# Optimization experiments

Hardware: AMD Instinct MI355X
Metric: run time of the kernel (lower is better)

Reference implementation:

```python
import jax, jax.numpy as jnp
import numpy as np

N_NODES = 50000
N_EDGES = 1600000
N_GRAPHS = 64
F_IN = 256
H = 1024
EPS = 1e-5


def setup_inputs() -> dict:
    key = jax.random.key(0)
    ks = jax.random.split(key, 6)
    x = jax.random.normal(ks[0], (N_NODES, F_IN), dtype=jnp.float32)
    edge_index = jax.random.randint(ks[1], (2, N_EDGES), 0, N_NODES, dtype=jnp.int32)
    batch = jnp.sort(jax.random.randint(ks[2], (N_NODES,), 0, N_GRAPHS, dtype=jnp.int32))
    # Glorot-ish init for GCN weights
    W0 = jax.random.normal(ks[3], (F_IN, H), dtype=jnp.float32) * (1.0 / np.sqrt(F_IN))
    b0 = jnp.zeros((H,), dtype=jnp.float32)
    Ws = jax.random.normal(ks[4], (3, H, H), dtype=jnp.float32) * (1.0 / np.sqrt(H))
    bs = jnp.zeros((3, H), dtype=jnp.float32)
    gammas = jnp.ones((4, H), dtype=jnp.float32)
    betas = jnp.zeros((4, H), dtype=jnp.float32)
    return {"x": x, "edge_index": edge_index, "batch": batch,
            "W0": W0, "b0": b0, "Ws": Ws, "bs": bs,
            "gammas": gammas, "betas": betas}


def _gcn_norm(edge_index, n_nodes):
    # Add self-loops (PyG GCNConv default), compute symmetric normalization.
    loops = jnp.arange(n_nodes, dtype=edge_index.dtype)
    row = jnp.concatenate([edge_index[0], loops])  # sources
    col = jnp.concatenate([edge_index[1], loops])  # targets (aggregation index)
    ones = jnp.ones(row.shape[0], dtype=jnp.float32)
    deg = jax.ops.segment_sum(ones, col, num_segments=n_nodes)
    dinv = jnp.where(deg > 0, jax.lax.rsqrt(deg), 0.0)
    norm = dinv[row] * dinv[col]  # [E + N]
    return row, col, norm


def _layer(h, W, b, gamma, beta, row, col, norm):
    ht = h @ W                                           # [N, H] GEMM
    msg = ht[row] * norm[:, None]                        # gather + scale
    agg = jax.ops.segment_sum(msg, col, num_segments=N_NODES) + b
    mu = jnp.mean(agg, axis=-1, keepdims=True)
    var = jnp.mean(jnp.square(agg - mu), axis=-1, keepdims=True)
    hn = (agg - mu) * jax.lax.rsqrt(var + EPS) * gamma + beta
    return jax.nn.relu(hn)


def reference(x, edge_index, batch, W0, b0, Ws, bs, gammas, betas):
    row, col, norm = _gcn_norm(edge_index, N_NODES)
    h = _layer(x, W0, b0, gammas[0], betas[0], row, col, norm)
    for i in range(3):
        h = _layer(h, Ws[i], bs[i], gammas[i + 1], betas[i + 1], row, col, norm)
    # scatter_mean over batch (graph-level pooling)
    sums = jax.ops.segment_sum(h, batch, num_segments=N_GRAPHS)
    cnt = jax.ops.segment_sum(jnp.ones((N_NODES,), jnp.float32), batch, num_segments=N_GRAPHS)
    return sums / jnp.maximum(cnt, 1.0)[:, None]
```

## Files before the change

### kernel.cpp

```cpp
#include <hip/hip_runtime.h>
#include <hip/hip_bf16.h>
#include <stdint.h>

#define NN 50000
#define NE 1600000
#define NG 64
#define FIN 256
#define HD 1024
#define EPSV 1e-5f

typedef __bf16 bf16;
typedef __bf16 bf16x4 __attribute__((ext_vector_type(4)));
typedef __bf16 bf16x8 __attribute__((ext_vector_type(8)));
typedef float f32x4 __attribute__((ext_vector_type(4)));

typedef const __attribute__((address_space(1))) void* gptr_as1;
typedef __attribute__((address_space(3))) void* lptr_as3;

__device__ __forceinline__ void load_g2l_16(const void* g, const void* l) {
  __builtin_amdgcn_global_load_lds((gptr_as1)(uintptr_t)g,
                                   (lptr_as3)(uint32_t)(uintptr_t)l, 16, 0, 0);
}

__global__ void hist_kernel(const int* __restrict__ col, int* __restrict__ cnt, int E) {
  int e = blockIdx.x * 256 + threadIdx.x;
  if (e < E) atomicAdd(&cnt[col[e]], 1);
}

__global__ void dinv_kernel(const int* __restrict__ cnt, float* __restrict__ dinv, int n) {
  int i = blockIdx.x * 256 + threadIdx.x;
  if (i < n) dinv[i] = rsqrtf((float)(cnt[i] + 1));
}

__global__ void scan_partial_kernel(const int* __restrict__ cnt, int* __restrict__ partial, int n) {
  __shared__ int red[4];
  int i = blockIdx.x * 256 + threadIdx.x;
  int v = (i < n) ? cnt[i] : 0;
  #pragma unroll
  for (int off = 32; off; off >>= 1) v += __shfl_down(v, off, 64);
  if ((threadIdx.x & 63) == 0) red[threadIdx.x >> 6] = v;
  __syncthreads();
  if (threadIdx.x == 0) partial[blockIdx.x] = red[0] + red[1] + red[2] + red[3];
}

__global__ void scan_scan_kernel(int* __restrict__ partial, int nb) {
  __shared__ int s[256];
  int t = threadIdx.x;
  int v = (t < nb) ? partial[t] : 0;
  s[t] = v;
  __syncthreads();
  for (int off = 1; off < 256; off <<= 1) {
    int x = (t >= off) ? s[t - off] : 0;
    __syncthreads();
    s[t] += x;
    __syncthreads();
  }
  if (t < nb) partial[t] = s[t] - v;
}

__global__ void scan_final_kernel(const int* __restrict__ cnt, const int* __restrict__ partial,
                                  int* __restrict__ row_ptr, int n, int E) {
  __shared__ int s[256];
  int t = threadIdx.x;
  int i = blockIdx.x * 256 + t;
  int v = (i < n) ? cnt[i] : 0;
  s[t] = v;
  __syncthreads();
  for (int off = 1; off < 256; off <<= 1) {
    int x = (t >= off) ? s[t - off] : 0;
    __syncthreads();
    s[t] += x;
    __syncthreads();
  }
  if (i < n) row_ptr[i] = partial[blockIdx.x] + s[t] - v;
  if (i == 0) row_ptr[n] = E;
}

__global__ void scatter_kernel(const int* __restrict__ rowi, const int* __restrict__ coli,
                               const int* __restrict__ row_ptr, int* __restrict__ fill,
                               const float* __restrict__ dinv,
                               int* __restrict__ csr_src, float* __restrict__ csr_w, int E) {
  int e = blockIdx.x * 256 + threadIdx.x;
  if (e >= E) return;
  int s = rowi[e], d = coli[e];
  int pos = row_ptr[d] + atomicAdd(&fill[d], 1);
  csr_src[pos] = s;
  csr_w[pos] = dinv[s] * dinv[d];
}

__global__ void cvt_kernel(const float* __restrict__ in, bf16* __restrict__ out, int n4) {
  int i = blockIdx.x * 256 + threadIdx.x;
  if (i >= n4) return;
  float4 v = ((const float4*)in)[i];
  bf16x4 o = { (bf16)v.x, (bf16)v.y, (bf16)v.z, (bf16)v.w };
  ((bf16x4*)out)[i] = o;
}

__global__ void transpose_w_kernel(const float* __restrict__ W, bf16* __restrict__ Wt,
                                   int K, int N) {
  __shared__ float tile[32][33];
  int n0 = blockIdx.x * 32, k0 = blockIdx.y * 32;
  int tx = threadIdx.x, ty = threadIdx.y;
  #pragma unroll
  for (int i = ty; i < 32; i += 8) tile[i][tx] = W[(size_t)(k0 + i) * N + n0 + tx];
  __syncthreads();
  #pragma unroll
  for (int i = ty; i < 32; i += 8) Wt[(size_t)(n0 + i) * K + k0 + tx] = (bf16)tile[tx][i];
}

__global__ __launch_bounds__(256, 2) void gemm_bt_q8_kernel(
    const bf16* __restrict__ A, const bf16* __restrict__ Bt,
    uint8_t* __restrict__ C8, float* __restrict__ scales, int M, int K) {
  __shared__ __align__(16) bf16 As[2][128 * 32];
  __shared__ __align__(16) bf16 Bs[2][128 * 32];
  __shared__ float smax[2][128];
  const int tid = threadIdx.x;
  const int w = tid >> 6, l = tid & 63;

  const int nwg = gridDim.x;
  const int o = blockIdx.x;
  const int lid = (o & 7) * (nwg >> 3) + (o >> 3);
  const int m0 = (lid >> 3) * 128, n0 = (lid & 7) * 128;
  const int cb = lid & 7;
  const int wr = w >> 1, wc = w & 1;

  f32x4 acc[4][4] = {};

  const int r0 = tid >> 2;
  const int c8 = (tid & 3) * 8;
  int ar0 = m0 + r0;       if (ar0 >= M) ar0 = M - 1;
  int ar1 = m0 + r0 + 64;  if (ar1 >= M) ar1 = M - 1;
  const bf16* a0 = A + (size_t)ar0 * K + c8;
  const bf16* a1 = A + (size_t)ar1 * K + c8;
  const bf16* b0 = Bt + (size_t)(n0 + r0) * K + c8;
  const bf16* b1 = Bt + (size_t)(n0 + r0 + 64) * K + c8;

  const int mrow = l & 15;
  const int kch = (l >> 4) * 8;

  auto stage = [&](int b, int k) {
    bf16* asw = &As[b][w * 512];
    bf16* bsw = &Bs[b][w * 512];
    load_g2l_16(a0 + k, asw);
    load_g2l_16(a1 + k, asw + 2048);
    load_g2l_16(b0 + k, bsw);
    load_g2l_16(b1 + k, bsw + 2048);
  };

  const int nit = K >> 5;
  stage(0, 0);
  __syncthreads();

  int cur = 0;
  for (int t = 0; t < nit; ++t) {
    if (t + 1 < nit) stage(cur ^ 1, (t + 1) << 5);
    bf16x8 af[4], bf_[4];
    #pragma unroll
    for (int m = 0; m < 4; m++)
      af[m] = *(const bf16x8*)&As[cur][(wr * 64 + m * 16 + mrow) * 32 + kch];
    #pragma unroll
    for (int n = 0; n < 4; n++)
      bf_[n] = *(const bf16x8*)&Bs[cur][(wc * 64 + n * 16 + mrow) * 32 + kch];
    #pragma unroll
    for (int m = 0; m < 4; m++)
      #pragma unroll
      for (int n = 0; n < 4; n++)
        acc[m][n] = __builtin_amdgcn_mfma_f32_16x16x32_bf16(af[m], bf_[n], acc[m][n], 0, 0, 0);
    __syncthreads();
    cur ^= 1;
  }

  float pmax[4][4];
  #pragma unroll
  for (int m = 0; m < 4; m++)
    #pragma unroll
    for (int r = 0; r < 4; r++) {
      float v = 0.f;
      #pragma unroll
      for (int n = 0; n < 4; n++) v = fmaxf(v, fabsf(acc[m][n][r]));
      #pragma unroll
      for (int mask = 1; mask < 16; mask <<= 1) v = fmaxf(v, __shfl_xor(v, mask, 64));
      pmax[m][r] = v;
    }
  if ((l & 15) == 0) {
    #pragma unroll
    for (int m = 0; m < 4; m++)
      #pragma unroll
      for (int r = 0; r < 4; r++)
        smax[wc][wr * 64 + m * 16 + (l >> 4) * 4 + r] = pmax[m][r];
  }
  __syncthreads();

  #pragma unroll
  for (int m = 0; m < 4; m++) {
    #pragma unroll
    for (int r = 0; r < 4; r++) {
      int rl = wr * 64 + m * 16 + (l >> 4) * 4 + r;
      int grow = m0 + rl;
      float mx = fmaxf(smax[0][rl], smax[1][rl]);
      float inv = (mx > 0.f) ? 127.0f / mx : 0.f;
      if (grow < M) {
        if (wc == 0 && (l & 15) == 0)
          scales[(size_t)grow * 8 + cb] = (mx > 0.f) ? mx / 127.0f : 0.f;
        #pragma unroll
        for (int n = 0; n < 4; n++) {
          int gcol = n0 + wc * 64 + n * 16 + (l & 15);
          int u = __float2int_rn(acc[m][n][r] * inv) + 128;
          C8[(size_t)grow * HD + gcol] = (uint8_t)u;
        }
      }
    }
  }
}

__device__ __forceinline__ void acc_u8(float acc[8], float& sw, float w, uint2 d) {
  sw += w;
  acc[0] += w * (float)(d.x & 0xffu);
  acc[1] += w * (float)((d.x >> 8) & 0xffu);
  acc[2] += w * (float)((d.x >> 16) & 0xffu);
  acc[3] += w * (float)(d.x >> 24);
  acc[4] += w * (float)(d.y & 0xffu);
  acc[5] += w * (float)((d.y >> 8) & 0xffu);
  acc[6] += w * (float)((d.y >> 16) & 0xffu);
  acc[7] += w * (float)(d.y >> 24);
}

__global__ __launch_bounds__(256) void agg_ln_u8_kernel(
    const uint8_t* __restrict__ htu8, const float* __restrict__ scales,
    const int* __restrict__ row_ptr,
    const int* __restrict__ csr_src, const float* __restrict__ csr_w,
    const float* __restrict__ dinv, const float* __restrict__ bias,
    const float* __restrict__ gamma, const float* __restrict__ beta,
    bf16* __restrict__ hout) {
  const int g = threadIdx.x >> 7;
  const int node = blockIdx.x * 2 + g;
  const int tt = threadIdx.x & 127;
  const int cbL = tt >> 4;
  const int wid = threadIdx.x >> 6;
  __shared__ float red[4];

  float acc[8] = {};
  float sw = 0.f;

  float dn = dinv[node];
  float wself = dn * dn * scales[(size_t)node * 8 + cbL];
  acc_u8(acc, sw, wself, ((const uint2*)(htu8 + (size_t)node * HD))[tt]);

  int e = row_ptr[node];
  const int e1 = row_ptr[node + 1];
  for (; e + 4 <= e1; e += 4) {
    int s0 = csr_src[e], s1 = csr_src[e + 1], s2 = csr_src[e + 2], s3 = csr_src[e + 3];
    float w0 = csr_w[e] * scales[(size_t)s0 * 8 + cbL];
    float w1 = csr_w[e + 1] * scales[(size_t)s1 * 8 + cbL];
    float w2 = csr_w[e + 2] * scales[(size_t)s2 * 8 + cbL];
    float w3 = csr_w[e + 3] * scales[(size_t)s3 * 8 + cbL];
    uint2 d0 = ((const uint2*)(htu8 + (size_t)s0 * HD))[tt];
    uint2 d1 = ((const uint2*)(htu8 + (size_t)s1 * HD))[tt];
    uint2 d2 = ((const uint2*)(htu8 + (size_t)s2 * HD))[tt];
    uint2 d3 = ((const uint2*)(htu8 + (size_t)s3 * HD))[tt];
    acc_u8(acc, sw, w0, d0);
    acc_u8(acc, sw, w1, d1);
    acc_u8(acc, sw, w2, d2);
    acc_u8(acc, sw, w3, d3);
  }
  for (; e < e1; e++) {
    int src = csr_src[e];
    float wgt = csr_w[e] * scales[(size_t)src * 8 + cbL];
    acc_u8(acc, sw, wgt, ((const uint2*)(htu8 + (size_t)src * HD))[tt]);
  }

  const float4* bias2 = (const float4*)bias;
  float4 ba = bias2[tt * 2], bb = bias2[tt * 2 + 1];
  float c128 = 128.0f * sw;
  acc[0] += ba.x - c128; acc[1] += ba.y - c128; acc[2] += ba.z - c128; acc[3] += ba.w - c128;
  acc[4] += bb.x - c128; acc[5] += bb.y - c128; acc[6] += bb.z - c128; acc[7] += bb.w - c128;

  float s = 0.f;
  #pragma unroll
  for (int j = 0; j < 8; j++) s += acc[j];
  #pragma unroll
  for (int off = 32; off; off >>= 1) s += __shfl_down(s, off, 64);
  if ((threadIdx.x & 63) == 0) red[wid] = s;
  __syncthreads();
  float mean = (red[g * 2] + red[g * 2 + 1]) * (1.0f / HD);
  __syncthreads();

  float d[8], s2 = 0.f;
  #pragma unroll
  for (int j = 0; j < 8; j++) { d[j] = acc[j] - mean; s2 += d[j] * d[j]; }
  #pragma unroll
  for (int off = 32; off; off >>= 1) s2 += __shfl_down(s2, off, 64);
  if ((threadIdx.x & 63) == 0) red[wid] = s2;
  __syncthreads();
  float var = (red[g * 2] + red[g * 2 + 1]) * (1.0f / HD);
  float rstd = rsqrtf(var + EPSV);

  const float4* gam2 = (const float4*)gamma;
  const float4* bet2 = (const float4*)beta;
  float4 g0 = gam2[tt * 2], g1 = gam2[tt * 2 + 1];
  float4 be0 = bet2[tt * 2], be1 = bet2[tt * 2 + 1];
  float gv[8] = {g0.x, g0.y, g0.z, g0.w, g1.x, g1.y, g1.z, g1.w};
  float bv[8] = {be0.x, be0.y, be0.z, be0.w, be1.x, be1.y, be1.z, be1.w};
  bf16x8 o;
  #pragma unroll
  for (int j = 0; j < 8; j++) o[j] = (bf16)fmaxf(d[j] * rstd * gv[j] + bv[j], 0.0f);
  ((bf16x8*)(hout + (size_t)node * HD))[tt] = o;
}

__global__ void starts_kernel(const int* __restrict__ batch, int* __restrict__ start,
                              int n, int ngraph) {
  int g = blockIdx.x * blockDim.x + threadIdx.x;
  if (g > ngraph) return;
  int lo = 0, hi = n;
  while (lo < hi) {
    int mid = (lo + hi) >> 1;
    if (batch[mid] < g) lo = mid + 1; else hi = mid;
  }
  start[g] = lo;
}

#define POOL_CHUNKS 8
__global__ void pool_partial_kernel(const bf16* __restrict__ h, const int* __restrict__ start,
                                    float* __restrict__ out) {
  int g = blockIdx.y, c = blockIdx.x;
  int t = threadIdx.x;
  int s0 = start[g], s1 = start[g + 1];
  int len = s1 - s0;
  int per = (len + POOL_CHUNKS - 1) / POOL_CHUNKS;
  int a = s0 + c * per;
  int b = min(a + per, s1);
  if (a >= b) return;
  f32x4 acc = {0.f, 0.f, 0.f, 0.f};
  for (int n = a; n < b; n++) {
    bf16x4 v = ((const bf16x4*)(h + (size_t)n * HD))[t];
    acc[0] += (float)v[0]; acc[1] += (float)v[1];
    acc[2] += (float)v[2]; acc[3] += (float)v[3];
  }
  float* o = out + (size_t)g * HD + t * 4;
  atomicAdd(o + 0, acc[0]);
  atomicAdd(o + 1, acc[1]);
  atomicAdd(o + 2, acc[2]);
  atomicAdd(o + 3, acc[3]);
}

__global__ void pool_div_kernel(float* __restrict__ out, const int* __restrict__ start) {
  int i = blockIdx.x * 256 + threadIdx.x;
  if (i >= NG * HD) return;
  int g = i >> 10;
  float c = (float)max(start[g + 1] - start[g], 1);
  out[i] = out[i] / c;
}

extern "C" void kernel_launch(void* const* d_in, const int* in_sizes, int n_in,
                              void* d_out, int out_size, void* d_ws, size_t ws_size,
                              hipStream_t stream) {
  const float* x      = (const float*)d_in[0];
  const int*   eidx   = (const int*)d_in[1];
  const int*   batch  = (const int*)d_in[2];
  const float* W0     = (const float*)d_in[3];
  const float* b0     = (const float*)d_in[4];
  const float* Ws     = (const float*)d_in[5];
  const float* bs     = (const float*)d_in[6];
  const float* gammas = (const float*)d_in[7];
  const float* betas  = (const float*)d_in[8];
  float* out = (float*)d_out;

  const int* erow = eidx;
  const int* ecol = eidx + NE;

  char* ws = (char*)d_ws;
  size_t off = 0;
  auto alloc = [&](size_t bytes) {
    void* p = ws + off;
    off = (off + bytes + 255) & ~(size_t)255;
    return p;
  };
  int*     cnt     = (int*)alloc((size_t)NN * 4);
  int*     row_ptr = (int*)alloc((size_t)(NN + 1) * 4);
  int*     fill    = (int*)alloc((size_t)NN * 4);
  int*     partial = (int*)alloc(256 * 4);
  float*   dinv    = (float*)alloc((size_t)NN * 4);
  int*     csr_src = (int*)alloc((size_t)NE * 4);
  float*   csr_w   = (float*)alloc((size_t)NE * 4);
  bf16*    Wt      = (bf16*)alloc((size_t)HD * HD * 2);
  bf16*    hbuf    = (bf16*)alloc((size_t)NN * HD * 2);
  uint8_t* ht8     = (uint8_t*)alloc((size_t)NN * HD);
  float*   scales  = (float*)alloc((size_t)NN * 8 * 4);
  int*     gstart  = (int*)alloc(65 * 4);

  hipMemsetAsync(cnt, 0, (size_t)NN * 4, stream);
  hipMemsetAsync(fill, 0, (size_t)NN * 4, stream);
  hipMemsetAsync(out, 0, (size_t)NG * HD * 4, stream);

  hist_kernel<<<(NE + 255) / 256, 256, 0, stream>>>(ecol, cnt, NE);
  dinv_kernel<<<(NN + 255) / 256, 256, 0, stream>>>(cnt, dinv, NN);
  int nb = (NN + 255) / 256;
  scan_partial_kernel<<<nb, 256, 0, stream>>>(cnt, partial, NN);
  scan_scan_kernel<<<1, 256, 0, stream>>>(partial, nb);
  scan_final_kernel<<<nb, 256, 0, stream>>>(cnt, partial, row_ptr, NN, NE);
  scatter_kernel<<<(NE + 255) / 256, 256, 0, stream>>>(erow, ecol, row_ptr, fill, dinv,
                                                       csr_src, csr_w, NE);
  starts_kernel<<<1, 128, 0, stream>>>(batch, gstart, NN, NG);

  cvt_kernel<<<(NN * FIN / 4 + 255) / 256, 256, 0, stream>>>(x, hbuf, NN * FIN / 4);

  const int nmt = (NN + 127) / 128;
  for (int L = 0; L < 4; L++) {
    int K = (L == 0) ? FIN : HD;
    const float* W    = (L == 0) ? W0 : Ws + (size_t)(L - 1) * HD * HD;
    const float* bias = (L == 0) ? b0 : bs + (size_t)(L - 1) * HD;
    transpose_w_kernel<<<dim3(HD / 32, K / 32), dim3(32, 8), 0, stream>>>(W, Wt, K, HD);
    gemm_bt_q8_kernel<<<nmt * 8, 256, 0, stream>>>(hbuf, Wt, ht8, scales, NN, K);
    agg_ln_u8_kernel<<<NN / 2, 256, 0, stream>>>(ht8, scales, row_ptr, csr_src, csr_w,
                                                 dinv, bias, gammas + (size_t)L * HD,
                                                 betas + (size_t)L * HD, hbuf);
  }

  pool_partial_kernel<<<dim3(POOL_CHUNKS, NG), 256, 0, stream>>>(hbuf, gstart, out);
  pool_div_kernel<<<(NG * HD + 255) / 256, 256, 0, stream>>>(out, gstart);
}
```

Before: 1.681 ms.

## Switch GEMM to int8 MFMA with per-row activation and per-column weight quantization

Quantizes input features, layer activations, and weights to int8, with per-row activation scales and per-column weight scales. The GEMM then runs on the i8 MFMA with int32 accumulation and is dequantized in the epilogue. The aggregation/LayerNorm kernel now emits int8 rows plus a scale, and pooling reads that format. This halves activation storage and traffic and uses the higher-throughput int8 matrix path, but adds extra weight-prep launches and accuracy risk from coarser quantization.

```diff
diff --git a/kernel.cpp b/kernel.cpp
--- a/kernel.cpp
+++ b/kernel.cpp
@@ -10,9 +10,8 @@
 #define EPSV 1e-5f
 
 typedef __bf16 bf16;
-typedef __bf16 bf16x4 __attribute__((ext_vector_type(4)));
-typedef __bf16 bf16x8 __attribute__((ext_vector_type(8)));
 typedef float f32x4 __attribute__((ext_vector_type(4)));
+typedef int i32x4 __attribute__((ext_vector_type(4)));
 
 typedef const __attribute__((address_space(1))) void* gptr_as1;
 typedef __attribute__((address_space(3))) void* lptr_as3;
@@ -88,16 +87,55 @@
   csr_w[pos] = dinv[s] * dinv[d];
 }
 
-__global__ void cvt_kernel(const float* __restrict__ in, bf16* __restrict__ out, int n4) {
-  int i = blockIdx.x * 256 + threadIdx.x;
-  if (i >= n4) return;
-  float4 v = ((const float4*)in)[i];
-  bf16x4 o = { (bf16)v.x, (bf16)v.y, (bf16)v.z, (bf16)v.w };
-  ((bf16x4*)out)[i] = o;
-}
-
-__global__ void transpose_w_kernel(const float* __restrict__ W, bf16* __restrict__ Wt,
-                                   int K, int N) {
+__global__ __launch_bounds__(256) void quant_x_kernel(const float* __restrict__ x,
+                                                      int8_t* __restrict__ A8,
+                                                      float* __restrict__ hscale) {
+  int row = blockIdx.x * 4 + (threadIdx.x >> 6);
+  int t = threadIdx.x & 63;
+  float4 v = ((const float4*)(x + (size_t)row * FIN))[t];
+  float m = fmaxf(fmaxf(fabsf(v.x), fabsf(v.y)), fmaxf(fabsf(v.z), fabsf(v.w)));
+  #pragma unroll
+  for (int off = 32; off; off >>= 1) m = fmaxf(m, __shfl_xor(m, off, 64));
+  float inv = (m > 0.f) ? 127.0f / m : 0.f;
+  int q0 = min(127, max(-127, __float2int_rn(v.x * inv)));
+  int q1 = min(127, max(-127, __float2int_rn(v.y * inv)));
+  int q2 = min(127, max(-127, __float2int_rn(v.z * inv)));
+  int q3 = min(127, max(-127, __float2int_rn(v.w * inv)));
+  uint32_t p = ((uint32_t)(q0 & 0xff)) | ((uint32_t)(q1 & 0xff) << 8) |
+               ((uint32_t)(q2 & 0xff) << 16) | ((uint32_t)(q3 & 0xff) << 24);
+  ((uint32_t*)A8)[(size_t)row * 64 + t] = p;
+  if (t == 0) hscale[row] = (m > 0.f) ? m / 127.0f : 0.f;
+}
+
+__global__ void wamax_kernel(const float* __restrict__ W, uint32_t* __restrict__ colmax,
+                             int K, int N) {
+  __shared__ float lds[8][32];
+  int n = blockIdx.x * 32 + threadIdx.x;
+  int k0 = blockIdx.y * 128;
+  int kend = min(k0 + 128, K);
+  float m = 0.f;
+  for (int k = k0 + threadIdx.y; k < kend; k += 8)
+    m = fmaxf(m, fabsf(W[(size_t)k * N + n]));
+  lds[threadIdx.y][threadIdx.x] = m;
+  __syncthreads();
+  if (threadIdx.y == 0) {
+    #pragma unroll
+    for (int i = 1; i < 8; i++) m = fmaxf(m, lds[i][threadIdx.x]);
+    atomicMax(&colmax[n], __float_as_uint(m));
+  }
+}
+
+__global__ void wscale_kernel(const uint32_t* __restrict__ colmax, float* __restrict__ wscale) {
+  int n = blockIdx.x * 256 + threadIdx.x;
+  if (n < HD) {
+    float m = __uint_as_float(colmax[n]);
+    wscale[n] = (m > 0.f) ? m / 127.0f : 0.f;
+  }
+}
+
+__global__ void transpose_wq8_kernel(const float* __restrict__ W,
+                                     const uint32_t* __restrict__ colmax,
+                                     int8_t* __restrict__ Wt8, int K, int N) {
   __shared__ float tile[32][33];
   int n0 = blockIdx.x * 32, k0 = blockIdx.y * 32;
   int tx = threadIdx.x, ty = threadIdx.y;
@@ -105,14 +143,20 @@
   for (int i = ty; i < 32; i += 8) tile[i][tx] = W[(size_t)(k0 + i) * N + n0 + tx];
   __syncthreads();
   #pragma unroll
-  for (int i = ty; i < 32; i += 8) Wt[(size_t)(n0 + i) * K + k0 + tx] = (bf16)tile[tx][i];
-}
-
-__global__ __launch_bounds__(256, 2) void gemm_bt_q8_kernel(
-    const bf16* __restrict__ A, const bf16* __restrict__ Bt,
+  for (int i = ty; i < 32; i += 8) {
+    float cm = __uint_as_float(colmax[n0 + i]);
+    float inv = (cm > 0.f) ? 127.0f / cm : 0.f;
+    int q = min(127, max(-127, __float2int_rn(tile[tx][i] * inv)));
+    Wt8[(size_t)(n0 + i) * K + k0 + tx] = (int8_t)q;
+  }
+}
+
+__global__ __launch_bounds__(256, 2) void gemm_i8_q8_kernel(
+    const int8_t* __restrict__ A8, const float* __restrict__ hscale,
+    const int8_t* __restrict__ Wt8, const float* __restrict__ wscale,
     uint8_t* __restrict__ C8, float* __restrict__ scales, int M, int K) {
-  __shared__ __align__(16) bf16 As[2][128 * 32];
-  __shared__ __align__(16) bf16 Bs[2][128 * 32];
+  __shared__ __align__(16) int8_t As[2][128 * 64];
+  __shared__ __align__(16) int8_t Bs[2][128 * 64];
   __shared__ float smax[2][128];
   const int tid = threadIdx.x;
   const int w = tid >> 6, l = tid & 63;
@@ -124,70 +168,75 @@
   const int cb = lid & 7;
   const int wr = w >> 1, wc = w & 1;
 
-  f32x4 acc[4][4] = {};
+  i32x4 acc[4][4] = {};
 
   const int r0 = tid >> 2;
-  const int c8 = (tid & 3) * 8;
+  const int c16 = (tid & 3) * 16;
   int ar0 = m0 + r0;       if (ar0 >= M) ar0 = M - 1;
   int ar1 = m0 + r0 + 64;  if (ar1 >= M) ar1 = M - 1;
-  const bf16* a0 = A + (size_t)ar0 * K + c8;
-  const bf16* a1 = A + (size_t)ar1 * K + c8;
-  const bf16* b0 = Bt + (size_t)(n0 + r0) * K + c8;
-  const bf16* b1 = Bt + (size_t)(n0 + r0 + 64) * K + c8;
+  const int8_t* a0 = A8 + (size_t)ar0 * K + c16;
+  const int8_t* a1 = A8 + (size_t)ar1 * K + c16;
+  const int8_t* b0 = Wt8 + (size_t)(n0 + r0) * K + c16;
+  const int8_t* b1 = Wt8 + (size_t)(n0 + r0 + 64) * K + c16;
 
   const int mrow = l & 15;
-  const int kch = (l >> 4) * 8;
+  const int kch = (l >> 4) * 16;
 
   auto stage = [&](int b, int k) {
-    bf16* asw = &As[b][w * 512];
-    bf16* bsw = &Bs[b][w * 512];
+    int8_t* asw = &As[b][w * 1024];
+    int8_t* bsw = &Bs[b][w * 1024];
     load_g2l_16(a0 + k, asw);
-    load_g2l_16(a1 + k, asw + 2048);
+    load_g2l_16(a1 + k, asw + 4096);
     load_g2l_16(b0 + k, bsw);
-    load_g2l_16(b1 + k, bsw + 2048);
+    load_g2l_16(b1 + k, bsw + 4096);
   };
 
-  const int nit = K >> 5;
+  const int nit = K >> 6;
   stage(0, 0);
   __syncthreads();
 
   int cur = 0;
   for (int t = 0; t < nit; ++t) {
-    if (t + 1 < nit) stage(cur ^ 1, (t + 1) << 5);
-    bf16x8 af[4], bf_[4];
+    if (t + 1 < nit) stage(cur ^ 1, (t + 1) << 6);
+    i32x4 af[4], bf_[4];
     #pragma unroll
     for (int m = 0; m < 4; m++)
-      af[m] = *(const bf16x8*)&As[cur][(wr * 64 + m * 16 + mrow) * 32 + kch];
+      af[m] = *(const i32x4*)&As[cur][(wr * 64 + m * 16 + mrow) * 64 + kch];
     #pragma unroll
     for (int n = 0; n < 4; n++)
-      bf_[n] = *(const bf16x8*)&Bs[cur][(wc * 64 + n * 16 + mrow) * 32 + kch];
+      bf_[n] = *(const i32x4*)&Bs[cur][(wc * 64 + n * 16 + mrow) * 64 + kch];
     #pragma unroll
     for (int m = 0; m < 4; m++)
       #pragma unroll
       for (int n = 0; n < 4; n++)
-        acc[m][n] = __builtin_amdgcn_mfma_f32_16x16x32_bf16(af[m], bf_[n], acc[m][n], 0, 0, 0);
+        acc[m][n] = __builtin_amdgcn_mfma_i32_16x16x64_i8(af[m], bf_[n], acc[m][n], 0, 0, 0);
     __syncthreads();
     cur ^= 1;
   }
 
-  float pmax[4][4];
-  #pragma unroll
-  for (int m = 0; m < 4; m++)
+  float wsv[4];
+  #pragma unroll
+  for (int n = 0; n < 4; n++) wsv[n] = wscale[n0 + wc * 64 + n * 16 + (l & 15)];
+
+  float cf[4][4][4];
+  #pragma unroll
+  for (int m = 0; m < 4; m++) {
     #pragma unroll
     for (int r = 0; r < 4; r++) {
+      int rl = wr * 64 + m * 16 + (l >> 4) * 4 + r;
+      int grow = m0 + rl; if (grow >= M) grow = M - 1;
+      float hs = hscale[grow];
       float v = 0.f;
       #pragma unroll
-      for (int n = 0; n < 4; n++) v = fmaxf(v, fabsf(acc[m][n][r]));
+      for (int n = 0; n < 4; n++) {
+        float c = (float)acc[m][n][r] * hs * wsv[n];
+        cf[m][n][r] = c;
+        v = fmaxf(v, fabsf(c));
+      }
       #pragma unroll
       for (int mask = 1; mask < 16; mask <<= 1) v = fmaxf(v, __shfl_xor(v, mask, 64));
-      pmax[m][r] = v;
+      if ((l & 15) == 0) smax[wc][rl] = v;
     }
-  if ((l & 15) == 0) {
-    #pragma unroll
-    for (int m = 0; m < 4; m++)
-      #pragma unroll
-      for (int r = 0; r < 4; r++)
-        smax[wc][wr * 64 + m * 16 + (l >> 4) * 4 + r] = pmax[m][r];
   }
   __syncthreads();
 
@@ -205,7 +254,7 @@
         #pragma unroll
         for (int n = 0; n < 4; n++) {
           int gcol = n0 + wc * 64 + n * 16 + (l & 15);
-          int u = __float2int_rn(acc[m][n][r] * inv) + 128;
+          int u = __float2int_rn(cf[m][n][r] * inv) + 128;
           C8[(size_t)grow * HD + gcol] = (uint8_t)u;
         }
       }
@@ -231,7 +280,7 @@
     const int* __restrict__ csr_src, const float* __restrict__ csr_w,
     const float* __restrict__ dinv, const float* __restrict__ bias,
     const float* __restrict__ gamma, const float* __restrict__ beta,
-    bf16* __restrict__ hout) {
+    int8_t* __restrict__ hq, float* __restrict__ hscale) {
   const int g = threadIdx.x >> 7;
   const int node = blockIdx.x * 2 + g;
   const int tt = threadIdx.x & 127;
@@ -301,10 +350,29 @@
   float4 be0 = bet2[tt * 2], be1 = bet2[tt * 2 + 1];
   float gv[8] = {g0.x, g0.y, g0.z, g0.w, g1.x, g1.y, g1.z, g1.w};
   float bv[8] = {be0.x, be0.y, be0.z, be0.w, be1.x, be1.y, be1.z, be1.w};
-  bf16x8 o;
-  #pragma unroll
-  for (int j = 0; j < 8; j++) o[j] = (bf16)fmaxf(d[j] * rstd * gv[j] + bv[j], 0.0f);
-  ((bf16x8*)(hout + (size_t)node * HD))[tt] = o;
+  float o[8];
+  float rmax = 0.f;
+  #pragma unroll
+  for (int j = 0; j < 8; j++) {
+    o[j] = fmaxf(d[j] * rstd * gv[j] + bv[j], 0.0f);
+    rmax = fmaxf(rmax, o[j]);
+  }
+
+  __syncthreads();
+  #pragma unroll
+  for (int off = 32; off; off >>= 1) rmax = fmaxf(rmax, __shfl_xor(rmax, off, 64));
+  if ((threadIdx.x & 63) == 0) red[wid] = rmax;
+  __syncthreads();
+  float rm = fmaxf(red[g * 2], red[g * 2 + 1]);
+  float qinv = (rm > 0.f) ? 127.0f / rm : 0.f;
+  int q[8];
+  #pragma unroll
+  for (int j = 0; j < 8; j++) q[j] = min(127, __float2int_rn(o[j] * qinv));
+  uint32_t p0 = ((uint32_t)q[0]) | ((uint32_t)q[1] << 8) | ((uint32_t)q[2] << 16) | ((uint32_t)q[3] << 24);
+  uint32_t p1 = ((uint32_t)q[4]) | ((uint32_t)q[5] << 8) | ((uint32_t)q[6] << 16) | ((uint32_t)q[7] << 24);
+  uint2 pk; pk.x = p0; pk.y = p1;
+  ((uint2*)(hq + (size_t)node * HD))[tt] = pk;
+  if (tt == 0) hscale[node] = (rm > 0.f) ? rm / 127.0f : 0.f;
 }
 
 __global__ void starts_kernel(const int* __restrict__ batch, int* __restrict__ start,
@@ -320,7 +388,9 @@
 }
 
 #define POOL_CHUNKS 8
-__global__ void pool_partial_kernel(const bf16* __restrict__ h, const int* __restrict__ start,
+__global__ void pool_partial_kernel(const int8_t* __restrict__ hq,
+                                    const float* __restrict__ hscale,
+                                    const int* __restrict__ start,
                                     float* __restrict__ out) {
   int g = blockIdx.y, c = blockIdx.x;
   int t = threadIdx.x;
@@ -332,9 +402,12 @@
   if (a >= b) return;
   f32x4 acc = {0.f, 0.f, 0.f, 0.f};
   for (int n = a; n < b; n++) {
-    bf16x4 v = ((const bf16x4*)(h + (size_t)n * HD))[t];
-    acc[0] += (float)v[0]; acc[1] += (float)v[1];
-    acc[2] += (float)v[2]; acc[3] += (float)v[3];
+    float hs = hscale[n];
+    uint32_t d = ((const uint32_t*)(hq + (size_t)n * HD))[t];
+    acc[0] += hs * (float)(d & 0xffu);
+    acc[1] += hs * (float)((d >> 8) & 0xffu);
+    acc[2] += hs * (float)((d >> 16) & 0xffu);
+    acc[3] += hs * (float)(d >> 24);
   }
   float* o = out + (size_t)g * HD + t * 4;
   atomicAdd(o + 0, acc[0]);
@@ -382,11 +455,15 @@
   float*   dinv    = (float*)alloc((size_t)NN * 4);
   int*     csr_src = (int*)alloc((size_t)NE * 4);
   float*   csr_w   = (float*)alloc((size_t)NE * 4);
-  bf16*    Wt      = (bf16*)alloc((size_t)HD * HD * 2);
-  bf16*    hbuf    = (bf16*)alloc((size_t)NN * HD * 2);
+  int8_t*  Wt8     = (int8_t*)alloc((size_t)HD * HD);
+  int8_t*  A8      = (int8_t*)alloc((size_t)NN * HD);
   uint8_t* ht8     = (uint8_t*)alloc((size_t)NN * HD);
   float*   scales  = (float*)alloc((size_t)NN * 8 * 4);
   int*     gstart  = (int*)alloc(65 * 4);
+
+  float*    wscale = (float*)cnt;
+  uint32_t* colmax = (uint32_t*)cnt + 1024;
+  float*    hscale = (float*)fill;
 
   hipMemsetAsync(cnt, 0, (size_t)NN * 4, stream);
   hipMemsetAsync(fill, 0, (size_t)NN * 4, stream);
@@ -402,20 +479,23 @@
                                                        csr_src, csr_w, NE);
   starts_kernel<<<1, 128, 0, stream>>>(batch, gstart, NN, NG);
 
-  cvt_kernel<<<(NN * FIN / 4 + 255) / 256, 256, 0, stream>>>(x, hbuf, NN * FIN / 4);
+  quant_x_kernel<<<NN / 4, 256, 0, stream>>>(x, A8, hscale);
 
   const int nmt = (NN + 127) / 128;
   for (int L = 0; L < 4; L++) {
     int K = (L == 0) ? FIN : HD;
     const float* W    = (L == 0) ? W0 : Ws + (size_t)(L - 1) * HD * HD;
     const float* bias = (L == 0) ? b0 : bs + (size_t)(L - 1) * HD;
-    transpose_w_kernel<<<dim3(HD / 32, K / 32), dim3(32, 8), 0, stream>>>(W, Wt, K, HD);
-    gemm_bt_q8_kernel<<<nmt * 8, 256, 0, stream>>>(hbuf, Wt, ht8, scales, NN, K);
+    hipMemsetAsync(colmax, 0, HD * 4, stream);
+    wamax_kernel<<<dim3(HD / 32, (K + 127) / 128), dim3(32, 8), 0, stream>>>(W, colmax, K, HD);
+    wscale_kernel<<<HD / 256, 256, 0, stream>>>(colmax, wscale);
+    transpose_wq8_kernel<<<dim3(HD / 32, K / 32), dim3(32, 8), 0, stream>>>(W, colmax, Wt8, K, HD);
+    gemm_i8_q8_kernel<<<nmt * 8, 256, 0, stream>>>(A8, hscale, Wt8, wscale, ht8, scales, NN, K);
     agg_ln_u8_kernel<<<NN / 2, 256, 0, stream>>>(ht8, scales, row_ptr, csr_src, csr_w,
                                                  dinv, bias, gammas + (size_t)L * HD,
-                                                 betas + (size_t)L * HD, hbuf);
-  }
-
-  pool_partial_kernel<<<dim3(POOL_CHUNKS, NG), 256, 0, stream>>>(hbuf, gstart, out);
+                                                 betas + (size_t)L * HD, A8, hscale);
+  }
+
+  pool_partial_kernel<<<dim3(POOL_CHUNKS, NG), 256, 0, stream>>>(A8, hscale, gstart, out);
   pool_div_kernel<<<(NG * HD + 255) / 256, 256, 0, stream>>>(out, gstart);
 }
```

Result: faster. 1.581 ms (-6.0%).
